# Kernel optimization log

Measured on AMD Instinct MI355X. Metric: run time of the kernel, lower is better.

Reference implementation:

```python
import jax, jax.numpy as jnp
import numpy as np
from jax import lax

B, T_ENC, T_DEC = 512, 64, 64
A = 64            # num_activities (pad token id = A)
ATTR_V = 10       # categorical attr vocab
ATTR_E, ACT_E, CF, ZD = 16, 64, 512, 128
TOT_ATTR = ATTR_E + 1           # 17
TDIM = TOT_ATTR // 2 + CF       # 8 + 512 = 520


def _lin(x, W, b):
    # torch nn.Linear: W is [out, in]
    return x @ W.T + b


def _cell(x, h, c, Wih, Whh, b):
    # torch LSTM cell, gate order i,f,g,o
    g = x @ Wih.T + h @ Whh.T + b
    i, f, gg, o = jnp.split(g, 4, axis=-1)
    c = jax.nn.sigmoid(f) * c + jax.nn.sigmoid(i) * jnp.tanh(gg)
    h = jax.nn.sigmoid(o) * jnp.tanh(c)
    return h, c


def setup_inputs() -> dict:
    key = jax.random.key(0)
    ks = iter(jax.random.split(key, 64))
    def n(shape, s=0.05):
        return jax.random.normal(next(ks), shape, jnp.float32) * s
    rng = np.random.default_rng(0)
    lens = rng.integers(2, T_ENC, size=B)
    acts_np = rng.integers(0, A - 1, size=(B, T_ENC))
    acts_np[np.arange(T_ENC)[None, :] >= lens[:, None]] = A  # pad token (max value -> argmax = len)
    return dict(
        attr_cat=jnp.asarray(rng.integers(0, ATTR_V, size=B), jnp.int32),
        attr_num=jax.random.uniform(next(ks), (B,), jnp.float32),
        acts=jnp.asarray(acts_np, jnp.int32),
        ts=jax.random.uniform(next(ks), (B, T_ENC), jnp.float32),
        epsilon=n((B, ZD), 1.0),
        attr_emb=n((ATTR_V, ATTR_E)),
        a2a_W=n((TOT_ATTR // 2, TOT_ATTR)), a2a_b=n((TOT_ATTR // 2,)),
        act_emb=n((A + 1, ACT_E)).at[A].set(0.0),  # padding_idx row zeroed
        eWih=n((4 * CF, ACT_E + 1)), eWhh=n((4 * CF, CF)), ebih=n((4 * CF,)), ebhh=n((4 * CF,)),
        mean_W=n((ZD, TDIM)), mean_b=n((ZD,)),
        var_W=n((ZD, TDIM)), var_b=n((ZD,)),
        z2t_W=n((TDIM, ZD)), z2t_b=n((TDIM,)),
        tc1_W=n((TDIM // 2, TDIM)), tc1_b=n((TDIM // 2,)),
        tc2_W=n((ATTR_V, TDIM // 2)), tc2_b=n((ATTR_V,)),
        tn1_W=n((TDIM // 2, TDIM)), tn1_b=n((TDIM // 2,)),
        tn2_W=n((1, TDIM // 2)), tn2_b=n((1,)),
        aWih=n((4 * CF, TDIM + ACT_E)), aWhh=n((4 * CF, CF)), abih=n((4 * CF,)), abhh=n((4 * CF,)),
        tWih=n((4 * CF, TDIM + ACT_E + 1)), tWhh=n((4 * CF, CF)), tbih=n((4 * CF,)), tbhh=n((4 * CF,)),
        e2act_W=n((A, CF)), e2act_b=n((A,)),
        ts1_W=n((CF // 2, CF)), ts1_b=n((CF // 2,)),
        ts2_W=n((1, CF // 2)), ts2_b=n((1,)),
    )


def reference(attr_cat, attr_num, acts, ts, epsilon,
              attr_emb, a2a_W, a2a_b, act_emb,
              eWih, eWhh, ebih, ebhh,
              mean_W, mean_b, var_W, var_b,
              z2t_W, z2t_b,
              tc1_W, tc1_b, tc2_W, tc2_b,
              tn1_W, tn1_b, tn2_W, tn2_b,
              aWih, aWhh, abih, abhh,
              tWih, tWhh, tbih, tbhh,
              e2act_W, e2act_b,
              ts1_W, ts1_b, ts2_W, ts2_b):
    # ---------- Encoder ----------
    e_attrs = jnp.concatenate([attr_emb[attr_cat], attr_num[:, None]], axis=1)   # [B,17]
    e_attrs = jax.nn.relu(_lin(e_attrs, a2a_W, a2a_b))                            # [B,8]
    x = jnp.concatenate([act_emb[acts], ts[:, :, None]], axis=2)                  # [B,T,ACT_E+1]
    eb = ebih + ebhh
    def enc_step(carry, xt):
        h, c = carry
        h, c = _cell(xt, h, c, eWih, eWhh, eb)
        return (h, c), h
    h0 = jnp.zeros((x.shape[0], CF), x.dtype)
    _, hs = lax.scan(enc_step, (h0, h0), jnp.swapaxes(x, 0, 1))
    cf_all = jnp.swapaxes(hs, 0, 1)                                               # [B,T,CF]
    # packed-sequence equivalence: LSTM is causal, we only read step lens-1
    lens = jnp.argmax(acts, axis=1)
    cf = cf_all[jnp.arange(cf_all.shape[0]), lens - 1]                            # [B,CF]
    t = jnp.concatenate([e_attrs, cf], axis=1)                                    # [B,TDIM]
    mean = _lin(t, mean_W, mean_b)
    var = _lin(t, var_W, var_b)
    z = mean + var * epsilon                                                      # reparameterization
    # ---------- Decoder ----------
    t_rec = jax.nn.relu(_lin(z, z2t_W, z2t_b))                                    # [B,TDIM]
    attr_cat_rec = jax.nn.softmax(_lin(jax.nn.relu(_lin(t_rec, tc1_W, tc1_b)), tc2_W, tc2_b), axis=1)
    attr_num_rec = jax.nn.sigmoid(_lin(jax.nn.relu(_lin(t_rec, tn1_W, tn1_b)), tn2_W, tn2_b))
    Bsz = t_rec.shape[0]
    ab, tb = abih + abhh, tbih + tbhh
    eot = jnp.broadcast_to(act_emb[A - 1], (Bsz, ACT_E))
    carry0 = (h0, h0, h0, h0, eot, jnp.zeros((Bsz, 1), t_rec.dtype))
    def dec_step(carry, _):
        h_a, c_a, h_t, c_t, ae, tsc = carry
        h_a, c_a = _cell(jnp.concatenate([t_rec, ae], 1), h_a, c_a, aWih, aWhh, ab)
        logits = _lin(h_a, e2act_W, e2act_b)                                      # [B,A]
        ae2 = act_emb[jnp.argmax(logits, axis=1)]                                 # greedy feedback
        h_t, c_t = _cell(jnp.concatenate([t_rec, ae2, tsc], 1), h_t, c_t, tWih, tWhh, tb)
        tsn = _lin(jax.nn.relu(_lin(h_t, ts1_W, ts1_b)), ts2_W, ts2_b)            # [B,1]
        return (h_a, c_a, h_t, c_t, ae2, tsn), (logits, tsn[:, 0])
    _, (logits_all, ts_all) = lax.scan(dec_step, carry0, None, length=T_DEC)
    acts_rec = jax.nn.softmax(jnp.swapaxes(logits_all, 0, 1), axis=2)             # [B,T_DEC,A]
    ts_rec = jnp.swapaxes(ts_all, 0, 1)                                           # [B,T_DEC]
    return (attr_cat_rec, attr_num_rec, acts_rec, ts_rec, mean, var)
```

## Files before the change

### kernel.cpp

```cpp
#include <hip/hip_runtime.h>
#include <math.h>


#define B 512
#define TT 64
#define CF 512
#define G4 2048
#define ZD 128
#define TDIM 520

typedef unsigned short u16;
typedef unsigned int u32;
typedef unsigned long long u64;
typedef short bf16x8 __attribute__((ext_vector_type(8)));
typedef float f32x4 __attribute__((ext_vector_type(4)));

__device__ __forceinline__ float sigm(float x) { return 1.f / (1.f + expf(-x)); }
__device__ __forceinline__ u16 f2bf(float f) {
    unsigned u = __float_as_uint(f);
    u += 0x7fffu + ((u >> 16) & 1u);
    return (u16)(u >> 16);
}
__device__ __forceinline__ float bf2f(u16 s) { return __uint_as_float(((unsigned)s) << 16); }
__device__ __forceinline__ u32 packbf(float v) {
    u16 hh = f2bf(v);
    u16 hl = f2bf(v - bf2f(hh));
    return (u32)hh | ((u32)hl << 16);
}

__device__ __forceinline__ void ast32(u32* p, u32 v) {
    __hip_atomic_store(p, v, __ATOMIC_RELAXED, __HIP_MEMORY_SCOPE_AGENT);
}
__device__ __forceinline__ u64 ald64(const u64* p) {
    return __hip_atomic_load(p, __ATOMIC_RELAXED, __HIP_MEMORY_SCOPE_AGENT);
}
__device__ __forceinline__ void astf(float* p, float v) {
    __hip_atomic_store(p, v, __ATOMIC_RELAXED, __HIP_MEMORY_SCOPE_AGENT);
}
__device__ __forceinline__ float aldf(const float* p) {
    return __hip_atomic_load(p, __ATOMIC_RELAXED, __HIP_MEMORY_SCOPE_AGENT);
}

__device__ __forceinline__ void unpk8(u64 a, u64 b, u64 c, u64 d,
                                      uint4& hi, uint4& lo) {
    u32 a0 = (u32)a, a1 = (u32)(a >> 32);
    u32 b0 = (u32)b, b1 = (u32)(b >> 32);
    u32 c0 = (u32)c, c1 = (u32)(c >> 32);
    u32 d0 = (u32)d, d1 = (u32)(d >> 32);
    hi.x = (a0 & 0xffffu) | (a1 << 16);  lo.x = (a0 >> 16) | (a1 & 0xffff0000u);
    hi.y = (b0 & 0xffffu) | (b1 << 16);  lo.y = (b0 >> 16) | (b1 & 0xffff0000u);
    hi.z = (c0 & 0xffffu) | (c1 << 16);  lo.z = (c0 >> 16) | (c1 & 0xffff0000u);
    hi.w = (d0 & 0xffffu) | (d1 << 16);  lo.w = (d0 >> 16) | (d1 & 0xffff0000u);
}

__device__ __forceinline__ void gsync_fast(int* bar, int target) {
    __syncthreads();
    if (threadIdx.x == 0) {
        __hip_atomic_fetch_add(bar, 1, __ATOMIC_RELEASE, __HIP_MEMORY_SCOPE_AGENT);
        while (__hip_atomic_load(bar, __ATOMIC_RELAXED, __HIP_MEMORY_SCOPE_AGENT) < target)
            __builtin_amdgcn_s_sleep(2);
    }
    __syncthreads();
}

__device__ __forceinline__ void gsync_full(int* bar, int target) {
    __syncthreads();
    if (threadIdx.x == 0) {
        __threadfence();
        __hip_atomic_fetch_add(bar, 1, __ATOMIC_ACQ_REL, __HIP_MEMORY_SCOPE_AGENT);
        while (__hip_atomic_load(bar, __ATOMIC_ACQUIRE, __HIP_MEMORY_SCOPE_AGENT) < target)
            __builtin_amdgcn_s_sleep(2);
        __threadfence();
    }
    __syncthreads();
}

struct __align__(16) GemmShared {
    u16 A[2][2][64][40];
    u16 Bw[2][2][64][40];
};

struct Pref { u64 a0, a1, a2, a3; uint4 bh, bl; };

template<int TERMS>
__device__ __forceinline__ void pf_issue(Pref& p, const u64* xp,
        const u16* wph, const u16* wpl, int it) {
    const int k = it << 5;
    const u64* xq = xp + (k >> 1);
    p.a0 = ald64(xq); p.a1 = ald64(xq + 1);
    p.a2 = ald64(xq + 2); p.a3 = ald64(xq + 3);
    p.bh = *(const uint4*)(wph + k);
    if (TERMS == 3) p.bl = *(const uint4*)(wpl + k);
}

template<int TERMS>
__device__ __forceinline__ void pf_write(GemmShared& sh, const Pref& p,
        int nxt, int srr, int skq) {
    uint4 hi, lo; unpk8(p.a0, p.a1, p.a2, p.a3, hi, lo);
    *(uint4*)&sh.A[nxt][0][srr][skq] = hi;
    *(uint4*)&sh.A[nxt][1][srr][skq] = lo;
    *(uint4*)&sh.Bw[nxt][0][srr][skq] = p.bh;
    if (TERMS == 3) *(uint4*)&sh.Bw[nxt][1][srr][skq] = p.bl;
}

template<int TERMS>
__device__ __forceinline__ void pf_comp(GemmShared& sh, int cur,
        int row, int ko, int fr, f32x4 acc[4]) {
    bf16x8 ah = *(const bf16x8*)&sh.A[cur][0][row][ko];
    bf16x8 al = *(const bf16x8*)&sh.A[cur][1][row][ko];
    #pragma unroll
    for (int nt = 0; nt < 4; ++nt) {
        bf16x8 bh = *(const bf16x8*)&sh.Bw[cur][0][(nt << 4) + fr][ko];
        acc[nt] = __builtin_amdgcn_mfma_f32_16x16x32_bf16(ah, bh, acc[nt], 0, 0, 0);
        if (TERMS == 3) {
            bf16x8 bl = *(const bf16x8*)&sh.Bw[cur][1][(nt << 4) + fr][ko];
            acc[nt] = __builtin_amdgcn_mfma_f32_16x16x32_bf16(ah, bl, acc[nt], 0, 0, 0);
        }
        acc[nt] = __builtin_amdgcn_mfma_f32_16x16x32_bf16(al, bh, acc[nt], 0, 0, 0);
    }
}

template<int TERMS>
__device__ __forceinline__ void gemm64i(
    GemmShared& sh,
    const u32* __restrict__ A32, int lda,
    const u16* __restrict__ Bh, const u16* __restrict__ Bl, int K, int ldb,
    f32x4 acc[4])
{
    const int tid = threadIdx.x;
    const int lane = tid & 63, ws = tid >> 6;
    const int fr = lane & 15, quad = lane >> 4, ko = quad << 3;
    const int srr = tid >> 2, skq = (tid & 3) << 3;
    const int row = (ws << 4) + fr;

    const u64* xp = (const u64*)(A32 + srr * lda + skq);
    const u16* wph = Bh + srr * ldb + skq;
    const u16* wpl = (TERMS == 3) ? (Bl + srr * ldb + skq) : (const u16*)0;

    const int niter = K >> 5;
    {
        u64 d0 = ald64(xp), d1 = ald64(xp + 1), d2 = ald64(xp + 2), d3 = ald64(xp + 3);
        uint4 hi, lo; unpk8(d0, d1, d2, d3, hi, lo);
        *(uint4*)&sh.A[0][0][srr][skq] = hi;
        *(uint4*)&sh.A[0][1][srr][skq] = lo;
        *(uint4*)&sh.Bw[0][0][srr][skq] = *(const uint4*)(wph);
        if (TERMS == 3) *(uint4*)&sh.Bw[0][1][srr][skq] = *(const uint4*)(wpl);
    }
    Pref pA, pB;
    if (niter > 1) pf_issue<TERMS>(pA, xp, wph, wpl, 1);
    if (niter > 2) pf_issue<TERMS>(pB, xp, wph, wpl, 2);
    __syncthreads();

    int i = 0;
    for (;;) {
        pf_comp<TERMS>(sh, 0, row, ko, fr, acc);
        if (i + 1 < niter) {
            pf_write<TERMS>(sh, pA, 1, srr, skq);
            if (i + 3 < niter) pf_issue<TERMS>(pA, xp, wph, wpl, i + 3);
        }
        __syncthreads();
        if (++i >= niter) break;
        pf_comp<TERMS>(sh, 1, row, ko, fr, acc);
        if (i + 1 < niter) {
            pf_write<TERMS>(sh, pB, 0, srr, skq);
            if (i + 3 < niter) pf_issue<TERMS>(pB, xp, wph, wpl, i + 3);
        }
        __syncthreads();
        if (++i >= niter) break;
    }
}

__device__ __forceinline__ void ts_strip(
    GemmShared& sh, const u32* __restrict__ Xt32r,
    const u16* __restrict__ W1h, const float* __restrict__ b1,
    const float* __restrict__ w2, int ncg, float s[4])
{
    const int lane = threadIdx.x & 63;
    const int fr = lane & 15;
    f32x4 ac[4] = {};
    gemm64i<2>(sh, Xt32r, 512, W1h + (size_t)(ncg << 6) * 512, nullptr, 512, 512, ac);
    s[0] = s[1] = s[2] = s[3] = 0.f;
    #pragma unroll
    for (int nt = 0; nt < 4; ++nt) {
        int j = (ncg << 6) + (nt << 4) + fr;
        float b1v = b1[j], w2v = w2[j];
        s[0] += fmaxf(ac[nt][0] + b1v, 0.f) * w2v;
        s[1] += fmaxf(ac[nt][1] + b1v, 0.f) * w2v;
        s[2] += fmaxf(ac[nt][2] + b1v, 0.f) * w2v;
        s[3] += fmaxf(ac[nt][3] + b1v, 0.f) * w2v;
    }
    #pragma unroll
    for (int off = 1; off < 16; off <<= 1) {
        s[0] += __shfl_xor(s[0], off);
        s[1] += __shfl_xor(s[1], off);
        s[2] += __shfl_xor(s[2], off);
        s[3] += __shfl_xor(s[3], off);
    }
}

__global__ __launch_bounds__(256, 1) void enc_coop(
    u32* __restrict__ Xe32,
    const u16* __restrict__ Weh, const u16* __restrict__ Wel,
    const float* __restrict__ biaspk,
    float* __restrict__ tcat, const int* __restrict__ lens,
    const int* __restrict__ acts, const float* __restrict__ tsv,
    const float* __restrict__ act_emb, int* __restrict__ bars)
{
    __shared__ GemmShared sh;
    const int bx = blockIdx.x, by = blockIdx.y, row0 = by << 6;
    const int tid = threadIdx.x, lane = tid & 63, ws = tid >> 6;
    const int fr = lane & 15, quad = lane >> 4;
    const int cell = (bx << 4) + fr;
    const int rbase = row0 + (ws << 4) + (quad << 2);
    int* bar = bars + by * 32;
    int gen = 0;

    float bb[4], ce[4] = {0.f, 0.f, 0.f, 0.f};
    int lm1[4];
    #pragma unroll
    for (int g = 0; g < 4; ++g) bb[g] = biaspk[(bx << 6) + (g << 4) + fr];
    #pragma unroll
    for (int r = 0; r < 4; ++r) lm1[r] = lens[rbase + r] - 1;

    for (int t = 0; t < TT; ++t) {
        const u32* xc = Xe32 + (size_t)(t & 1) * B * 608;
        u32* xn = Xe32 + (size_t)((t + 1) & 1) * B * 608;

        f32x4 acc[4] = {};
        gemm64i<3>(sh, xc + (size_t)row0 * 608, 608,
                   Weh + (size_t)(bx << 6) * 608, Wel + (size_t)(bx << 6) * 608,
                   608, 608, acc);

        #pragma unroll
        for (int r = 0; r < 4; ++r) {
            int b = rbase + r;
            float gi = acc[0][r] + bb[0], gf = acc[1][r] + bb[1];
            float gg = acc[2][r] + bb[2], go = acc[3][r] + bb[3];
            float cn = sigm(gf) * ce[r] + sigm(gi) * tanhf(gg);
            ce[r] = cn;
            float h = sigm(go) * tanhf(cn);
            ast32(&xn[b * 608 + 65 + cell], packbf(h));
            if (t == lm1[r]) tcat[b * TDIM + 8 + cell] = h;
        }
        if (t < TT - 1) {
            for (int idx = tid; idx < 130; idx += 256) {
                int hi2 = (idx >= 65);
                int r = (bx << 1) + hi2, cc = idx - hi2 * 65;
                int b = row0 + r;
                float v = (cc < 64) ? act_emb[acts[(b << 6) + t + 1] * 64 + cc]
                                    : tsv[(b << 6) + t + 1];
                ast32(&xn[b * 608 + cc], packbf(v));
            }
            gsync_fast(bar, (++gen) * 32);
        }
    }
}

__global__ __launch_bounds__(256, 1) void dec_coop(
    u32* __restrict__ Xa32,
    u16* Wah, u16* Wal,
    const float* __restrict__ aWih, const float* __restrict__ aWhh,
    const float* __restrict__ base_a,
    u32* __restrict__ Xt32,
    const u16* __restrict__ Wth, const u16* __restrict__ Wtl,
    const float* __restrict__ base_t,
    const u16* __restrict__ E2h, const u16* __restrict__ E2l,
    const float* __restrict__ e2b, const float* __restrict__ act_emb,
    float* __restrict__ out_acts, float* __restrict__ out_ts,
    const u16* __restrict__ W1h, const float* __restrict__ b1,
    const float* __restrict__ w2, const float* __restrict__ b2p,
    float* __restrict__ tspart, int* __restrict__ bars)
{
    __shared__ GemmShared sh;
    __shared__ u16 ae2h[64][72];
    __shared__ u16 ae2l[64][72];
    const int bx = blockIdx.x, by = blockIdx.y, row0 = by << 6;
    const int tid = threadIdx.x, lane = tid & 63, ws = tid >> 6;
    const int fr = lane & 15, quad = lane >> 4;
    const int srr = tid >> 2, skq = (tid & 3) << 3;
    const bool bx0 = (bx == 0);
    const int cell = (bx << 4) + fr;
    const int rb0 = (ws << 4) + (quad << 2);
    const int rbase = row0 + rb0;
    const float tsb2 = b2p[0];
    int* barG = bars + 512;
    int* bar  = bars + 256 + by * 32;
    int gen = 0;

    {
        const int gtid = (((by << 5) + bx) << 8) + tid;
        for (int idx = gtid; idx < G4 * 576; idx += 32 * 8 * 256) {
            int np = idx / 576, k = idx - np * 576;
            int g = (np & 63) >> 4;
            int n = (g << 9) + (((np >> 6) << 4) + (np & 15));
            float v = (k < 64) ? aWih[n * 584 + 520 + k] : aWhh[(n << 9) + k - 64];
            u16 h = f2bf(v);
            Wah[idx] = h; Wal[idx] = f2bf(v - bf2f(h));
        }
    }

    float e2bv[4];
    float ca_r[4] = {0.f, 0.f, 0.f, 0.f}, ct_r[4] = {0.f, 0.f, 0.f, 0.f};
    #pragma unroll
    for (int nt = 0; nt < 4; ++nt) e2bv[nt] = e2b[(nt << 4) + fr];

    gsync_full(barG, 256);

    for (int t = 0; t < TT; ++t) {
        u32* xac = Xa32 + (size_t)(t & 1) * B * 576;
        u32* xan = Xa32 + (size_t)((t + 1) & 1) * B * 576;
        const u32* xtc = Xt32 + (size_t)(t & 1) * B * 512;
        u32* xtn = Xt32 + (size_t)((t + 1) & 1) * B * 512;

        {
            f32x4 acc[4] = {};
            gemm64i<3>(sh, xac + (size_t)row0 * 576, 576,
                       Wah + (size_t)(bx << 6) * 576, Wal + (size_t)(bx << 6) * 576,
                       576, 576, acc);
            #pragma unroll
            for (int r = 0; r < 4; ++r) {
                int b = rbase + r;
                const float* bp = base_a + (size_t)b * G4 + (bx << 6) + fr;
                float gi = acc[0][r] + bp[0], gf = acc[1][r] + bp[16];
                float gg = acc[2][r] + bp[32], go = acc[3][r] + bp[48];
                float cn = sigm(gf) * ca_r[r] + sigm(gi) * tanhf(gg);
                ca_r[r] = cn;
                float h = sigm(go) * tanhf(cn);
                ast32(&xan[b * 576 + 64 + cell], packbf(h));
            }
            if (bx < 4 && t > 0) {
                float s[4];
                ts_strip(sh, xtc + (size_t)row0 * 512, W1h, b1, w2, bx, s);
                if (fr == 0) {
                    #pragma unroll
                    for (int r = 0; r < 4; ++r) astf(&tspart[(bx << 9) + rbase + r], s[r]);
                }
            }
        }
        gsync_fast(bar, (++gen) * 32);

        if (t > 0 && bx == 1 && tid < 64) {
            int b = row0 + tid;
            out_ts[(b << 6) + t - 1] =
                aldf(&tspart[b]) + aldf(&tspart[512 + b]) +
                aldf(&tspart[1024 + b]) + aldf(&tspart[1536 + b]) + tsb2;
        }
        float tsq = 0.f;
        if (t > 0) {
            int b = row0 + srr;
            tsq = aldf(&tspart[b]) + aldf(&tspart[512 + b]) +
                  aldf(&tspart[1024 + b]) + aldf(&tspart[1536 + b]) + tsb2;
        }
        {
            f32x4 acc[4] = {};
            gemm64i<3>(sh, xan + (size_t)row0 * 576 + 64, 576, E2h, E2l, 512, 512, acc);
            #pragma unroll
            for (int r = 0; r < 4; ++r) {
                float l0 = acc[0][r] + e2bv[0], l1 = acc[1][r] + e2bv[1];
                float l2 = acc[2][r] + e2bv[2], l3 = acc[3][r] + e2bv[3];
                float m = fmaxf(fmaxf(l0, l1), fmaxf(l2, l3));
                #pragma unroll
                for (int off = 1; off < 16; off <<= 1) m = fmaxf(m, __shfl_xor(m, off));
                float e0 = expf(l0 - m), e1 = expf(l1 - m);
                float e2v = expf(l2 - m), e3 = expf(l3 - m);
                float sm = e0 + e1 + e2v + e3;
                #pragma unroll
                for (int off = 1; off < 16; off <<= 1) sm += __shfl_xor(sm, off);
                float bv = l0; int bc = fr;
                if (l1 > bv) { bv = l1; bc = 16 + fr; }
                if (l2 > bv) { bv = l2; bc = 32 + fr; }
                if (l3 > bv) { bv = l3; bc = 48 + fr; }
                #pragma unroll
                for (int off = 1; off < 16; off <<= 1) {
                    float ov = __shfl_xor(bv, off);
                    int oc = __shfl_xor(bc, off);
                    if (ov > bv || (ov == bv && oc < bc)) { bv = ov; bc = oc; }
                }
                int rl = rb0 + r, b = row0 + rl;
                if (bx0) {
                    float inv = 1.f / sm;
                    float* op = out_acts + (((size_t)(b << 6) + t) << 6);
                    op[fr] = e0 * inv; op[16 + fr] = e1 * inv;
                    op[32 + fr] = e2v * inv; op[48 + fr] = e3 * inv;
                }
                #pragma unroll
                for (int ci = 0; ci < 4; ++ci) {
                    int cc = (fr << 2) + ci;
                    float v = act_emb[(bc << 6) + cc];
                    u16 hh = f2bf(v), hl = f2bf(v - bf2f(hh));
                    ae2h[rl][cc] = hh; ae2l[rl][cc] = hl;
                    if (bx0) ast32(&xan[b * 576 + cc], ((u32)hh) | ((u32)hl << 16));
                }
            }
        }
        __syncthreads();

        f32x4 acc[4] = {};
        gemm64i<3>(sh, xtc + (size_t)row0 * 512, 512,
                   Wth + (size_t)(bx << 6) * 608, Wtl + (size_t)(bx << 6) * 608,
                   512, 608, acc);
        {
            const u16* wph = Wth + (size_t)((bx << 6) + srr) * 608 + skq;
            const u16* wpl = Wtl + (size_t)((bx << 6) + srr) * 608 + skq;
            const int ko = quad << 3;
            for (int i = 16; i < 19; ++i) {
                int k0 = i << 5;
                uint4 vh, vl;
                if (i < 18) {
                    int co = k0 - 512 + skq;
                    vh = *(const uint4*)&ae2h[srr][co];
                    vl = *(const uint4*)&ae2l[srr][co];
                } else {
                    union U { uint4 q; u16 s[8]; } uh, ul;
                    uh.q = make_uint4(0, 0, 0, 0); ul.q = make_uint4(0, 0, 0, 0);
                    if (skq == 0) {
                        u16 hh = f2bf(tsq);
                        uh.s[0] = hh; ul.s[0] = f2bf(tsq - bf2f(hh));
                    }
                    vh = uh.q; vl = ul.q;
                }
                uint4 wh = *(const uint4*)(wph + k0);
                uint4 wl = *(const uint4*)(wpl + k0);
                __syncthreads();
                *(uint4*)&sh.A[0][0][srr][skq] = vh;
                *(uint4*)&sh.A[0][1][srr][skq] = vl;
                *(uint4*)&sh.Bw[0][0][srr][skq] = wh;
                *(uint4*)&sh.Bw[0][1][srr][skq] = wl;
                __syncthreads();
                bf16x8 ah = *(const bf16x8*)&sh.A[0][0][(ws << 4) + fr][ko];
                bf16x8 al = *(const bf16x8*)&sh.A[0][1][(ws << 4) + fr][ko];
                #pragma unroll
                for (int nt = 0; nt < 4; ++nt) {
                    bf16x8 bh = *(const bf16x8*)&sh.Bw[0][0][(nt << 4) + fr][ko];
                    bf16x8 bl = *(const bf16x8*)&sh.Bw[0][1][(nt << 4) + fr][ko];
                    acc[nt] = __builtin_amdgcn_mfma_f32_16x16x32_bf16(ah, bh, acc[nt], 0, 0, 0);
                    acc[nt] = __builtin_amdgcn_mfma_f32_16x16x32_bf16(ah, bl, acc[nt], 0, 0, 0);
                    acc[nt] = __builtin_amdgcn_mfma_f32_16x16x32_bf16(al, bh, acc[nt], 0, 0, 0);
                }
            }
        }
        #pragma unroll
        for (int r = 0; r < 4; ++r) {
            int b = rbase + r;
            const float* bp = base_t + (size_t)b * G4 + (bx << 6) + fr;
            float gi = acc[0][r] + bp[0], gf = acc[1][r] + bp[16];
            float gg = acc[2][r] + bp[32], go = acc[3][r] + bp[48];
            float cn = sigm(gf) * ct_r[r] + sigm(gi) * tanhf(gg);
            ct_r[r] = cn;
            float h = sigm(go) * tanhf(cn);
            ast32(&xtn[(b << 9) + cell], packbf(h));
        }
        gsync_fast(bar, (++gen) * 32);
    }

    if (bx < 4) {
        float s[4];
        ts_strip(sh, Xt32 + (size_t)row0 * 512, W1h, b1, w2, bx, s);
        if (fr == 0) {
            #pragma unroll
            for (int r = 0; r < 4; ++r) astf(&tspart[(bx << 9) + rbase + r], s[r]);
        }
    }
    gsync_fast(bar, (++gen) * 32);
    if (bx == 0 && tid < 64) {
        int b = row0 + tid;
        out_ts[(b << 6) + 63] =
            aldf(&tspart[b]) + aldf(&tspart[512 + b]) +
            aldf(&tspart[1024 + b]) + aldf(&tspart[1536 + b]) + tsb2;
    }
}

__device__ __forceinline__ int perm_src(int np) {
    int g = (np & 63) >> 4;
    int cell = ((np >> 6) << 4) + (np & 15);
    return (g << 9) + cell;
}

__global__ __launch_bounds__(256) void gemm_tn(
    const float* __restrict__ A, const float* __restrict__ Am,
    const float* __restrict__ Av, const float* __restrict__ Ae, int lda,
    const float* __restrict__ W1p, int ldw1,
    const float* __restrict__ W2p, int ldw2,
    int N, int K,
    const float* __restrict__ b1p, const float* __restrict__ b2p,
    float* __restrict__ C1, float* __restrict__ C2, int ldc,
    int relu, int permW)
{
    const float* W = W1p; int ldw = ldw1;
    const float* bias = b1p; float* C = C1;
    if (blockIdx.z == 1) { W = W2p; ldw = ldw2; bias = b2p; C = C2; }

    __shared__ __align__(16) float As[32][68];
    __shared__ __align__(16) float Ws[32][68];
    const int tid = threadIdx.x;
    const int tx = tid & 15, ty = tid >> 4;
    const int row0 = blockIdx.y << 6;
    const int col0 = blockIdx.x << 6;

    float acc[4][4] = {};

    for (int k0 = 0; k0 < K; k0 += 32) {
        #pragma unroll
        for (int s = 0; s < 2; ++s) {
            int f = tid + (s << 8);
            int rr = f >> 3;
            int kq = (f & 7) << 2;
            int k = k0 + kq;
            float4 v = make_float4(0.f, 0.f, 0.f, 0.f);
            size_t ro = (size_t)(row0 + rr) * (size_t)lda;
            if (Am) {
                if (k + 3 < K) {
                    float4 m = *(const float4*)(Am + ro + k);
                    float4 vv = *(const float4*)(Av + ro + k);
                    float4 e = *(const float4*)(Ae + ro + k);
                    v.x = fmaf(vv.x, e.x, m.x); v.y = fmaf(vv.y, e.y, m.y);
                    v.z = fmaf(vv.z, e.z, m.z); v.w = fmaf(vv.w, e.w, m.w);
                } else {
                    if (k + 0 < K) v.x = fmaf(Av[ro + k], Ae[ro + k], Am[ro + k]);
                    if (k + 1 < K) v.y = fmaf(Av[ro + k + 1], Ae[ro + k + 1], Am[ro + k + 1]);
                    if (k + 2 < K) v.z = fmaf(Av[ro + k + 2], Ae[ro + k + 2], Am[ro + k + 2]);
                }
            } else {
                const float* ap = A + ro;
                if (k + 3 < K) v = *(const float4*)(ap + k);
                else {
                    if (k + 0 < K) v.x = ap[k + 0];
                    if (k + 1 < K) v.y = ap[k + 1];
                    if (k + 2 < K) v.z = ap[k + 2];
                }
            }
            As[kq + 0][rr] = v.x; As[kq + 1][rr] = v.y;
            As[kq + 2][rr] = v.z; As[kq + 3][rr] = v.w;
        }
        #pragma unroll
        for (int s = 0; s < 2; ++s) {
            int f = tid + (s << 8);
            int rr = f >> 3;
            int kq = (f & 7) << 2;
            int k = k0 + kq;
            int n = col0 + rr;
            float4 v = make_float4(0.f, 0.f, 0.f, 0.f);
            if (n < N) {
                int nsrc = permW ? perm_src(n) : n;
                const float* wp = W + (size_t)nsrc * (size_t)ldw;
                if (k + 3 < K) v = *(const float4*)(wp + k);
                else {
                    if (k + 0 < K) v.x = wp[k + 0];
                    if (k + 1 < K) v.y = wp[k + 1];
                    if (k + 2 < K) v.z = wp[k + 2];
                }
            }
            Ws[kq + 0][rr] = v.x; Ws[kq + 1][rr] = v.y;
            Ws[kq + 2][rr] = v.z; Ws[kq + 3][rr] = v.w;
        }
        __syncthreads();
        #pragma unroll
        for (int k = 0; k < 32; ++k) {
            float4 av = *(const float4*)&As[k][ty << 2];
            float4 bv = *(const float4*)&Ws[k][tx << 2];
            acc[0][0] = fmaf(av.x, bv.x, acc[0][0]);
            acc[0][1] = fmaf(av.x, bv.y, acc[0][1]);
            acc[0][2] = fmaf(av.x, bv.z, acc[0][2]);
            acc[0][3] = fmaf(av.x, bv.w, acc[0][3]);
            acc[1][0] = fmaf(av.y, bv.x, acc[1][0]);
            acc[1][1] = fmaf(av.y, bv.y, acc[1][1]);
            acc[1][2] = fmaf(av.y, bv.z, acc[1][2]);
            acc[1][3] = fmaf(av.y, bv.w, acc[1][3]);
            acc[2][0] = fmaf(av.z, bv.x, acc[2][0]);
            acc[2][1] = fmaf(av.z, bv.y, acc[2][1]);
            acc[2][2] = fmaf(av.z, bv.z, acc[2][2]);
            acc[2][3] = fmaf(av.z, bv.w, acc[2][3]);
            acc[3][0] = fmaf(av.w, bv.x, acc[3][0]);
            acc[3][1] = fmaf(av.w, bv.y, acc[3][1]);
            acc[3][2] = fmaf(av.w, bv.z, acc[3][2]);
            acc[3][3] = fmaf(av.w, bv.w, acc[3][3]);
        }
        __syncthreads();
    }

    #pragma unroll
    for (int i = 0; i < 4; ++i) {
        int rr = row0 + (ty << 2) + i;
        float* cp = C + (size_t)rr * (size_t)ldc;
        #pragma unroll
        for (int j = 0; j < 4; ++j) {
            int cc = col0 + (tx << 2) + j;
            if (cc < N) {
                float v = acc[i][j];
                if (bias) v += bias[cc];
                if (relu) v = fmaxf(v, 0.f);
                cp[cc] = v;
            }
        }
    }
}

#define N_WE (G4 * 608)
#define N_WT (G4 * 608)
#define N_W1 (256 * 512)
#define N_E2 (64 * 512)
__global__ void pack_all(
    u16* __restrict__ Weh, u16* __restrict__ Wel,
    u16* __restrict__ Wth, u16* __restrict__ Wtl,
    u16* __restrict__ W1h,
    u16* __restrict__ E2h, u16* __restrict__ E2l,
    float* __restrict__ be, float* __restrict__ ba, float* __restrict__ bt,
    const float* __restrict__ eWih, const float* __restrict__ eWhh,
    const float* __restrict__ tWih, const float* __restrict__ tWhh,
    const float* __restrict__ ts1W, const float* __restrict__ e2W,
    const float* __restrict__ ebih, const float* __restrict__ ebhh,
    const float* __restrict__ abih, const float* __restrict__ abhh,
    const float* __restrict__ tbih, const float* __restrict__ tbhh)
{
    int idx = blockIdx.x * 256 + threadIdx.x;
    if (idx < N_WE) {
        int np = idx / 608, k = idx - np * 608;
        int n = perm_src(np);
        float v = 0.f;
        if (k < 65) v = eWih[n * 65 + k];
        else if (k < 577) v = eWhh[(n << 9) + k - 65];
        u16 h = f2bf(v); Weh[idx] = h; Wel[idx] = f2bf(v - bf2f(h));
        return;
    }
    idx -= N_WE;
    if (idx < N_WT) {
        int np = idx / 608, k = idx - np * 608;
        int n = perm_src(np);
        float v = 0.f;
        if (k < 512) v = tWhh[(n << 9) + k];
        else if (k < 576) v = tWih[n * 585 + 520 + (k - 512)];
        else if (k == 576) v = tWih[n * 585 + 584];
        u16 h = f2bf(v); Wth[idx] = h; Wtl[idx] = f2bf(v - bf2f(h));
        return;
    }
    idx -= N_WT;
    if (idx < N_W1) {
        W1h[idx] = f2bf(ts1W[idx]);
        return;
    }
    idx -= N_W1;
    if (idx < N_E2) {
        float v = e2W[idx];
        u16 h = f2bf(v); E2h[idx] = h; E2l[idx] = f2bf(v - bf2f(h));
        return;
    }
    idx -= N_E2;
    if (idx < G4) {
        int n = perm_src(idx);
        be[idx] = ebih[n] + ebhh[n];
        ba[idx] = abih[n] + abhh[n];
        bt[idx] = tbih[n] + tbhh[n];
    }
}

__global__ __launch_bounds__(256) void init_all(
    u32* __restrict__ xe0, u32* __restrict__ xe1,
    int* __restrict__ lens, float* __restrict__ tcat,
    u32* __restrict__ xa0, u32* __restrict__ xt0,
    const int* __restrict__ acts, const float* __restrict__ tsv,
    const float* __restrict__ act_emb,
    const int* __restrict__ attr_cat, const float* __restrict__ attr_num,
    const float* __restrict__ attr_emb,
    const float* __restrict__ a2aW, const float* __restrict__ a2ab,
    int* __restrict__ bars)
{
    int b = blockIdx.x, tid = threadIdx.x;
    if (b == 0) {
        for (int j = tid; j < 1024; j += 256)
            __hip_atomic_store(&bars[j], 0, __ATOMIC_RELAXED, __HIP_MEMORY_SCOPE_AGENT);
    }
    for (int j = tid; j < 608; j += 256) {
        float v = 0.f;
        if (j < 64) v = act_emb[acts[b << 6] * 64 + j];
        else if (j == 64) v = tsv[b << 6];
        xe0[b * 608 + j] = packbf(v);
        if (j >= 577) xe1[b * 608 + j] = 0;
    }
    for (int j = tid; j < CF; j += 256) {
        xt0[(b << 9) + j] = 0;
    }
    for (int j = tid; j < 576; j += 256) {
        float v = (j < 64) ? act_emb[63 * 64 + j] : 0.f;
        xa0[b * 576 + j] = packbf(v);
    }
    if (tid < 64) {
        int v = acts[(b << 6) + tid];
        int m = v;
        #pragma unroll
        for (int off = 32; off; off >>= 1) m = max(m, __shfl_xor(m, off));
        unsigned long long mask = __ballot(v == m);
        if (tid == 0) lens[b] = __ffsll(mask) - 1;
    }
    if (tid < 8) {
        const float* wr = a2aW + tid * 17;
        const float* em = attr_emb + attr_cat[b] * 16;
        float s = a2ab[tid];
        #pragma unroll
        for (int k = 0; k < 16; ++k) s = fmaf(em[k], wr[k], s);
        s = fmaf(attr_num[b], wr[16], s);
        tcat[b * TDIM + tid] = fmaxf(s, 0.f);
    }
}

__global__ __launch_bounds__(64) void attr_heads(
    const float* __restrict__ hid1, const float* __restrict__ hid2,
    const float* __restrict__ tc2W, const float* __restrict__ tc2b,
    const float* __restrict__ tn2W, const float* __restrict__ tn2b,
    float* __restrict__ out_cat, float* __restrict__ out_num) {
    __shared__ __align__(16) float h1[260], h2[260], sl[10];
    int b = blockIdx.x, tid = threadIdx.x;
    for (int k = tid; k < 260; k += 64) {
        h1[k] = hid1[b * 260 + k];
        h2[k] = hid2[b * 260 + k];
    }
    __syncthreads();
    if (tid < 10) {
        float l = tc2b[tid];
        const float* wr = tc2W + tid * 260;
        for (int k = 0; k < 260; ++k) l = fmaf(h1[k], wr[k], l);
        sl[tid] = l;
    }
    __syncthreads();
    if (tid < 10) {
        float m = sl[0];
        for (int i = 1; i < 10; ++i) m = fmaxf(m, sl[i]);
        float ssum = 0.f;
        for (int i = 0; i < 10; ++i) ssum += expf(sl[i] - m);
        out_cat[b * 10 + tid] = expf(sl[tid] - m) / ssum;
    }
    float p = 0.f;
    for (int k = tid; k < 260; k += 64) p = fmaf(h2[k], tn2W[k], p);
    #pragma unroll
    for (int off = 32; off; off >>= 1) p += __shfl_xor(p, off);
    if (tid == 0) out_num[b] = 1.f / (1.f + expf(-(p + tn2b[0])));
}

extern "C" void kernel_launch(void* const* d_in, const int* in_sizes, int n_in,
                              void* d_out, int out_size, void* d_ws, size_t ws_size,
                              hipStream_t stream) {
    const int*   attr_cat = (const int*)  d_in[0];
    const float* attr_num = (const float*)d_in[1];
    const int*   acts     = (const int*)  d_in[2];
    const float* tsv      = (const float*)d_in[3];
    const float* eps      = (const float*)d_in[4];
    const float* attr_emb = (const float*)d_in[5];
    const float* a2a_W    = (const float*)d_in[6];
    const float* a2a_b    = (const float*)d_in[7];
    const float* act_emb  = (const float*)d_in[8];
    const float* eWih     = (const float*)d_in[9];
    const float* eWhh     = (const float*)d_in[10];
    const float* ebih     = (const float*)d_in[11];
    const float* ebhh     = (const float*)d_in[12];
    const float* mean_W   = (const float*)d_in[13];
    const float* mean_b   = (const float*)d_in[14];
    const float* var_W    = (const float*)d_in[15];
    const float* var_b    = (const float*)d_in[16];
    const float* z2t_W    = (const float*)d_in[17];
    const float* z2t_b    = (const float*)d_in[18];
    const float* tc1_W    = (const float*)d_in[19];
    const float* tc1_b    = (const float*)d_in[20];
    const float* tc2_W    = (const float*)d_in[21];
    const float* tc2_b    = (const float*)d_in[22];
    const float* tn1_W    = (const float*)d_in[23];
    const float* tn1_b    = (const float*)d_in[24];
    const float* tn2_W    = (const float*)d_in[25];
    const float* tn2_b    = (const float*)d_in[26];
    const float* aWih     = (const float*)d_in[27];
    const float* aWhh     = (const float*)d_in[28];
    const float* abih     = (const float*)d_in[29];
    const float* abhh     = (const float*)d_in[30];
    const float* tWih     = (const float*)d_in[31];
    const float* tWhh     = (const float*)d_in[32];
    const float* tbih     = (const float*)d_in[33];
    const float* tbhh     = (const float*)d_in[34];
    const float* e2act_W  = (const float*)d_in[35];
    const float* e2act_b  = (const float*)d_in[36];
    const float* ts1_W    = (const float*)d_in[37];
    const float* ts1_b    = (const float*)d_in[38];
    const float* ts2_W    = (const float*)d_in[39];
    const float* ts2_b    = (const float*)d_in[40];

    float* out = (float*)d_out;
    float* out_cat  = out;
    float* out_num  = out + 5120;
    float* out_acts = out + 5632;
    float* out_ts   = out + 2102784;
    float* outm     = out + 2135552;
    float* outv     = out + 2201088;

    char* w = (char*)d_ws;
    auto alloc = [&](size_t bytes) { char* p = w; w += (bytes + 255) & ~(size_t)255; return p; };
    u16*   Wt_hi  = (u16*)alloc((size_t)G4 * 608 * 2);
    u16*   Wt_lo  = (u16*)alloc((size_t)G4 * 608 * 2);
    u16*   W1h    = (u16*)alloc(256 * 512 * 2);
    u16*   E2h    = (u16*)alloc(64 * 512 * 2);
    u16*   E2l    = (u16*)alloc(64 * 512 * 2);
    float* bias_e = (float*)alloc(G4 * 4);
    float* bias_a = (float*)alloc(G4 * 4);
    float* bias_t = (float*)alloc(G4 * 4);
    float* base_a = (float*)alloc((size_t)B * G4 * 4);
    float* base_t = (float*)alloc((size_t)B * G4 * 4);
    u32*   Xa32   = (u32*)alloc((size_t)2 * B * 576 * 4);
    u32*   Xt32   = (u32*)alloc((size_t)2 * B * 512 * 4);
    float* tcat   = (float*)alloc((size_t)B * TDIM * 4);
    float* t_rec  = (float*)alloc((size_t)B * TDIM * 4);
    float* hid1   = (float*)alloc((size_t)B * 260 * 4);
    float* hid2   = (float*)alloc((size_t)B * 260 * 4);
    int*   lens   = (int*)alloc(512 * 4);
    float* partial4 = (float*)alloc(4 * 512 * 4);
    int*   bars   = (int*)alloc(4096);
    char* phase = w;
    u16*   We_hi  = (u16*)(phase);
    u16*   We_lo  = (u16*)(phase + (size_t)G4 * 608 * 2);
    u32*   Xe32   = (u32*)(phase + (size_t)2 * G4 * 608 * 2);
    u16*   Wa_hi  = (u16*)(phase);
    u16*   Wa_lo  = (u16*)(phase + (size_t)G4 * 576 * 2);
    (void)ws_size; (void)in_sizes; (void)n_in; (void)out_size;

    {
        int total = N_WE + N_WT + N_W1 + N_E2 + G4;
        pack_all<<<(total + 255) / 256, 256, 0, stream>>>(
            We_hi, We_lo, Wt_hi, Wt_lo, W1h, E2h, E2l,
            bias_e, bias_a, bias_t,
            eWih, eWhh, tWih, tWhh, ts1_W, e2act_W,
            ebih, ebhh, abih, abhh, tbih, tbhh);
    }
    init_all<<<B, 256, 0, stream>>>(
        Xe32, Xe32 + (size_t)B * 608,
        lens, tcat, Xa32, Xt32,
        acts, tsv, act_emb, attr_cat, attr_num, attr_emb, a2a_W, a2a_b,
        bars);

    enc_coop<<<dim3(32, 8), 256, 0, stream>>>(
        Xe32, We_hi, We_lo, bias_e, tcat, lens, acts, tsv, act_emb,
        bars);

    gemm_tn<<<dim3(2, 8, 2), 256, 0, stream>>>(
        tcat, nullptr, nullptr, nullptr, TDIM, mean_W, TDIM, var_W, TDIM,
        ZD, TDIM, mean_b, var_b, outm, outv, ZD, 0, 0);
    gemm_tn<<<dim3(9, 8, 1), 256, 0, stream>>>(
        nullptr, outm, outv, eps, ZD, z2t_W, ZD, nullptr, 0,
        TDIM, ZD, z2t_b, nullptr, t_rec, nullptr, TDIM, 1, 0);
    gemm_tn<<<dim3(5, 8, 2), 256, 0, stream>>>(
        t_rec, nullptr, nullptr, nullptr, TDIM, tc1_W, TDIM, tn1_W, TDIM,
        260, TDIM, tc1_b, tn1_b, hid1, hid2, 260, 1, 0);
    attr_heads<<<B, 64, 0, stream>>>(hid1, hid2, tc2_W, tc2_b, tn2_W, tn2_b, out_cat, out_num);
    gemm_tn<<<dim3(32, 8, 2), 256, 0, stream>>>(
        t_rec, nullptr, nullptr, nullptr, TDIM, aWih, 584, tWih, 585,
        G4, TDIM, bias_a, bias_t, base_a, base_t, G4, 0, 1);

    dec_coop<<<dim3(32, 8), 256, 0, stream>>>(
        Xa32, Wa_hi, Wa_lo, aWih, aWhh, base_a,
        Xt32, Wt_hi, Wt_lo, base_t,
        E2h, E2l, e2act_b, act_emb, out_acts, out_ts,
        W1h, ts1_b, ts2_W, ts2_b, partial4,
        bars);
}
```

Baseline: 4.904 ms.

## Split coop kernels into producer and consumer warps for GEMM tile loads

Doubles the block size of the encoder and decoder cooperative kernels to 512 threads. The upper 256 threads only load global tiles into shared memory and the lower 256 only run MFMA and the LSTM epilogues, so loading and compute are specialised by warp. The aim is to hide global load latency behind the matrix math in the per-step recurrent GEMMs. It costs extra warps and registers per block, and the double-buffer synchronisation is unchanged, so the overlap gained may be limited.

```diff
diff --git a/kernel.cpp b/kernel.cpp
--- a/kernel.cpp
+++ b/kernel.cpp
@@ -128,9 +128,11 @@
     f32x4 acc[4])
 {
     const int tid = threadIdx.x;
-    const int lane = tid & 63, ws = tid >> 6;
+    const bool cons = tid < 256;
+    const int lane = tid & 63, ws = (tid >> 6) & 3;
     const int fr = lane & 15, quad = lane >> 4, ko = quad << 3;
-    const int srr = tid >> 2, skq = (tid & 3) << 3;
+    const int ptid = tid & 255;
+    const int srr = ptid >> 2, skq = (ptid & 3) << 3;
     const int row = (ws << 4) + fr;
 
     const u64* xp = (const u64*)(A32 + srr * lda + skq);
@@ -138,30 +140,32 @@
     const u16* wpl = (TERMS == 3) ? (Bl + srr * ldb + skq) : (const u16*)0;
 
     const int niter = K >> 5;
-    {
+    Pref pA, pB;
+    if (!cons) {
         u64 d0 = ald64(xp), d1 = ald64(xp + 1), d2 = ald64(xp + 2), d3 = ald64(xp + 3);
         uint4 hi, lo; unpk8(d0, d1, d2, d3, hi, lo);
         *(uint4*)&sh.A[0][0][srr][skq] = hi;
         *(uint4*)&sh.A[0][1][srr][skq] = lo;
         *(uint4*)&sh.Bw[0][0][srr][skq] = *(const uint4*)(wph);
         if (TERMS == 3) *(uint4*)&sh.Bw[0][1][srr][skq] = *(const uint4*)(wpl);
-    }
-    Pref pA, pB;
-    if (niter > 1) pf_issue<TERMS>(pA, xp, wph, wpl, 1);
-    if (niter > 2) pf_issue<TERMS>(pB, xp, wph, wpl, 2);
+        if (niter > 1) pf_issue<TERMS>(pA, xp, wph, wpl, 1);
+        if (niter > 2) pf_issue<TERMS>(pB, xp, wph, wpl, 2);
+    }
     __syncthreads();
 
     int i = 0;
     for (;;) {
-        pf_comp<TERMS>(sh, 0, row, ko, fr, acc);
-        if (i + 1 < niter) {
+        if (cons) {
+            pf_comp<TERMS>(sh, 0, row, ko, fr, acc);
+        } else if (i + 1 < niter) {
             pf_write<TERMS>(sh, pA, 1, srr, skq);
             if (i + 3 < niter) pf_issue<TERMS>(pA, xp, wph, wpl, i + 3);
         }
         __syncthreads();
         if (++i >= niter) break;
-        pf_comp<TERMS>(sh, 1, row, ko, fr, acc);
-        if (i + 1 < niter) {
+        if (cons) {
+            pf_comp<TERMS>(sh, 1, row, ko, fr, acc);
+        } else if (i + 1 < niter) {
             pf_write<TERMS>(sh, pB, 0, srr, skq);
             if (i + 3 < niter) pf_issue<TERMS>(pB, xp, wph, wpl, i + 3);
         }
@@ -180,25 +184,27 @@
     f32x4 ac[4] = {};
     gemm64i<2>(sh, Xt32r, 512, W1h + (size_t)(ncg << 6) * 512, nullptr, 512, 512, ac);
     s[0] = s[1] = s[2] = s[3] = 0.f;
-    #pragma unroll
-    for (int nt = 0; nt < 4; ++nt) {
-        int j = (ncg << 6) + (nt << 4) + fr;
-        float b1v = b1[j], w2v = w2[j];
-        s[0] += fmaxf(ac[nt][0] + b1v, 0.f) * w2v;
-        s[1] += fmaxf(ac[nt][1] + b1v, 0.f) * w2v;
-        s[2] += fmaxf(ac[nt][2] + b1v, 0.f) * w2v;
-        s[3] += fmaxf(ac[nt][3] + b1v, 0.f) * w2v;
-    }
-    #pragma unroll
-    for (int off = 1; off < 16; off <<= 1) {
-        s[0] += __shfl_xor(s[0], off);
-        s[1] += __shfl_xor(s[1], off);
-        s[2] += __shfl_xor(s[2], off);
-        s[3] += __shfl_xor(s[3], off);
-    }
-}
-
-__global__ __launch_bounds__(256, 1) void enc_coop(
+    if (threadIdx.x < 256) {
+        #pragma unroll
+        for (int nt = 0; nt < 4; ++nt) {
+            int j = (ncg << 6) + (nt << 4) + fr;
+            float b1v = b1[j], w2v = w2[j];
+            s[0] += fmaxf(ac[nt][0] + b1v, 0.f) * w2v;
+            s[1] += fmaxf(ac[nt][1] + b1v, 0.f) * w2v;
+            s[2] += fmaxf(ac[nt][2] + b1v, 0.f) * w2v;
+            s[3] += fmaxf(ac[nt][3] + b1v, 0.f) * w2v;
+        }
+        #pragma unroll
+        for (int off = 1; off < 16; off <<= 1) {
+            s[0] += __shfl_xor(s[0], off);
+            s[1] += __shfl_xor(s[1], off);
+            s[2] += __shfl_xor(s[2], off);
+            s[3] += __shfl_xor(s[3], off);
+        }
+    }
+}
+
+__global__ __launch_bounds__(512, 1) void enc_coop(
     u32* __restrict__ Xe32,
     const u16* __restrict__ Weh, const u16* __restrict__ Wel,
     const float* __restrict__ biaspk,
@@ -208,7 +214,9 @@
 {
     __shared__ GemmShared sh;
     const int bx = blockIdx.x, by = blockIdx.y, row0 = by << 6;
-    const int tid = threadIdx.x, lane = tid & 63, ws = tid >> 6;
+    const int tid = threadIdx.x;
+    const bool cons = tid < 256;
+    const int lane = tid & 63, ws = (tid >> 6) & 3;
     const int fr = lane & 15, quad = lane >> 4;
     const int cell = (bx << 4) + fr;
     const int rbase = row0 + (ws << 4) + (quad << 2);
@@ -231,19 +239,21 @@
                    Weh + (size_t)(bx << 6) * 608, Wel + (size_t)(bx << 6) * 608,
                    608, 608, acc);
 
-        #pragma unroll
-        for (int r = 0; r < 4; ++r) {
-            int b = rbase + r;
-            float gi = acc[0][r] + bb[0], gf = acc[1][r] + bb[1];
-            float gg = acc[2][r] + bb[2], go = acc[3][r] + bb[3];
-            float cn = sigm(gf) * ce[r] + sigm(gi) * tanhf(gg);
-            ce[r] = cn;
-            float h = sigm(go) * tanhf(cn);
-            ast32(&xn[b * 608 + 65 + cell], packbf(h));
-            if (t == lm1[r]) tcat[b * TDIM + 8 + cell] = h;
+        if (cons) {
+            #pragma unroll
+            for (int r = 0; r < 4; ++r) {
+                int b = rbase + r;
+                float gi = acc[0][r] + bb[0], gf = acc[1][r] + bb[1];
+                float gg = acc[2][r] + bb[2], go = acc[3][r] + bb[3];
+                float cn = sigm(gf) * ce[r] + sigm(gi) * tanhf(gg);
+                ce[r] = cn;
+                float h = sigm(go) * tanhf(cn);
+                ast32(&xn[b * 608 + 65 + cell], packbf(h));
+                if (t == lm1[r]) tcat[b * TDIM + 8 + cell] = h;
+            }
         }
         if (t < TT - 1) {
-            for (int idx = tid; idx < 130; idx += 256) {
+            for (int idx = tid; idx < 130; idx += 512) {
                 int hi2 = (idx >= 65);
                 int r = (bx << 1) + hi2, cc = idx - hi2 * 65;
                 int b = row0 + r;
@@ -256,7 +266,7 @@
     }
 }
 
-__global__ __launch_bounds__(256, 1) void dec_coop(
+__global__ __launch_bounds__(512, 1) void dec_coop(
     u32* __restrict__ Xa32,
     u16* Wah, u16* Wal,
     const float* __restrict__ aWih, const float* __restrict__ aWhh,
@@ -275,9 +285,12 @@
     __shared__ u16 ae2h[64][72];
     __shared__ u16 ae2l[64][72];
     const int bx = blockIdx.x, by = blockIdx.y, row0 = by << 6;
-    const int tid = threadIdx.x, lane = tid & 63, ws = tid >> 6;
+    const int tid = threadIdx.x;
+    const bool cons = tid < 256;
+    const int lane = tid & 63, ws = (tid >> 6) & 3;
     const int fr = lane & 15, quad = lane >> 4;
-    const int srr = tid >> 2, skq = (tid & 3) << 3;
+    const int ptid = tid & 255;
+    const int srr = ptid >> 2, skq = (ptid & 3) << 3;
     const bool bx0 = (bx == 0);
     const int cell = (bx << 4) + fr;
     const int rb0 = (ws << 4) + (quad << 2);
@@ -288,8 +301,8 @@
     int gen = 0;
 
     {
-        const int gtid = (((by << 5) + bx) << 8) + tid;
-        for (int idx = gtid; idx < G4 * 576; idx += 32 * 8 * 256) {
+        const int gtid = (((by << 5) + bx) << 9) + tid;
+        for (int idx = gtid; idx < G4 * 576; idx += 32 * 8 * 512) {
             int np = idx / 576, k = idx - np * 576;
             int g = (np & 63) >> 4;
             int n = (g << 9) + (((np >> 6) << 4) + (np & 15));
@@ -317,21 +330,23 @@
             gemm64i<3>(sh, xac + (size_t)row0 * 576, 576,
                        Wah + (size_t)(bx << 6) * 576, Wal + (size_t)(bx << 6) * 576,
                        576, 576, acc);
-            #pragma unroll
-            for (int r = 0; r < 4; ++r) {
-                int b = rbase + r;
-                const float* bp = base_a + (size_t)b * G4 + (bx << 6) + fr;
-                float gi = acc[0][r] + bp[0], gf = acc[1][r] + bp[16];
-                float gg = acc[2][r] + bp[32], go = acc[3][r] + bp[48];
-                float cn = sigm(gf) * ca_r[r] + sigm(gi) * tanhf(gg);
-                ca_r[r] = cn;
-                float h = sigm(go) * tanhf(cn);
-                ast32(&xan[b * 576 + 64 + cell], packbf(h));
+            if (cons) {
+                #pragma unroll
+                for (int r = 0; r < 4; ++r) {
+                    int b = rbase + r;
+                    const float* bp = base_a + (size_t)b * G4 + (bx << 6) + fr;
+                    float gi = acc[0][r] + bp[0], gf = acc[1][r] + bp[16];
+                    float gg = acc[2][r] + bp[32], go = acc[3][r] + bp[48];
+                    float cn = sigm(gf) * ca_r[r] + sigm(gi) * tanhf(gg);
+                    ca_r[r] = cn;
+                    float h = sigm(go) * tanhf(cn);
+                    ast32(&xan[b * 576 + 64 + cell], packbf(h));
+                }
             }
             if (bx < 4 && t > 0) {
                 float s[4];
                 ts_strip(sh, xtc + (size_t)row0 * 512, W1h, b1, w2, bx, s);
-                if (fr == 0) {
+                if (cons && fr == 0) {
                     #pragma unroll
                     for (int r = 0; r < 4; ++r) astf(&tspart[(bx << 9) + rbase + r], s[r]);
                 }
@@ -354,42 +369,44 @@
         {
             f32x4 acc[4] = {};
             gemm64i<3>(sh, xan + (size_t)row0 * 576 + 64, 576, E2h, E2l, 512, 512, acc);
-            #pragma unroll
-            for (int r = 0; r < 4; ++r) {
-                float l0 = acc[0][r] + e2bv[0], l1 = acc[1][r] + e2bv[1];
-                float l2 = acc[2][r] + e2bv[2], l3 = acc[3][r] + e2bv[3];
-                float m = fmaxf(fmaxf(l0, l1), fmaxf(l2, l3));
+            if (cons) {
                 #pragma unroll
-                for (int off = 1; off < 16; off <<= 1) m = fmaxf(m, __shfl_xor(m, off));
-                float e0 = expf(l0 - m), e1 = expf(l1 - m);
-                float e2v = expf(l2 - m), e3 = expf(l3 - m);
-                float sm = e0 + e1 + e2v + e3;
-                #pragma unroll
-                for (int off = 1; off < 16; off <<= 1) sm += __shfl_xor(sm, off);
-                float bv = l0; int bc = fr;
-                if (l1 > bv) { bv = l1; bc = 16 + fr; }
-                if (l2 > bv) { bv = l2; bc = 32 + fr; }
-                if (l3 > bv) { bv = l3; bc = 48 + fr; }
-                #pragma unroll
-                for (int off = 1; off < 16; off <<= 1) {
-                    float ov = __shfl_xor(bv, off);
-                    int oc = __shfl_xor(bc, off);
-                    if (ov > bv || (ov == bv && oc < bc)) { bv = ov; bc = oc; }
-                }
-                int rl = rb0 + r, b = row0 + rl;
-                if (bx0) {
-                    float inv = 1.f / sm;
-                    float* op = out_acts + (((size_t)(b << 6) + t) << 6);
-                    op[fr] = e0 * inv; op[16 + fr] = e1 * inv;
-                    op[32 + fr] = e2v * inv; op[48 + fr] = e3 * inv;
-                }
-                #pragma unroll
-                for (int ci = 0; ci < 4; ++ci) {
-                    int cc = (fr << 2) + ci;
-                    float v = act_emb[(bc << 6) + cc];
-                    u16 hh = f2bf(v), hl = f2bf(v - bf2f(hh));
-                    ae2h[rl][cc] = hh; ae2l[rl][cc] = hl;
-                    if (bx0) ast32(&xan[b * 576 + cc], ((u32)hh) | ((u32)hl << 16));
+                for (int r = 0; r < 4; ++r) {
+                    float l0 = acc[0][r] + e2bv[0], l1 = acc[1][r] + e2bv[1];
+                    float l2 = acc[2][r] + e2bv[2], l3 = acc[3][r] + e2bv[3];
+                    float m = fmaxf(fmaxf(l0, l1), fmaxf(l2, l3));
+                    #pragma unroll
+                    for (int off = 1; off < 16; off <<= 1) m = fmaxf(m, __shfl_xor(m, off));
+                    float e0 = expf(l0 - m), e1 = expf(l1 - m);
+                    float e2v = expf(l2 - m), e3 = expf(l3 - m);
+                    float sm = e0 + e1 + e2v + e3;
+                    #pragma unroll
+                    for (int off = 1; off < 16; off <<= 1) sm += __shfl_xor(sm, off);
+                    float bv = l0; int bc = fr;
+                    if (l1 > bv) { bv = l1; bc = 16 + fr; }
+                    if (l2 > bv) { bv = l2; bc = 32 + fr; }
+                    if (l3 > bv) { bv = l3; bc = 48 + fr; }
+                    #pragma unroll
+                    for (int off = 1; off < 16; off <<= 1) {
+                        float ov = __shfl_xor(bv, off);
+                        int oc = __shfl_xor(bc, off);
+                        if (ov > bv || (ov == bv && oc < bc)) { bv = ov; bc = oc; }
+                    }
+                    int rl = rb0 + r, b = row0 + rl;
+                    if (bx0) {
+                        float inv = 1.f / sm;
+                        float* op = out_acts + (((size_t)(b << 6) + t) << 6);
+                        op[fr] = e0 * inv; op[16 + fr] = e1 * inv;
+                        op[32 + fr] = e2v * inv; op[48 + fr] = e3 * inv;
+                    }
+                    #pragma unroll
+                    for (int ci = 0; ci < 4; ++ci) {
+                        int cc = (fr << 2) + ci;
+                        float v = act_emb[(bc << 6) + cc];
+                        u16 hh = f2bf(v), hl = f2bf(v - bf2f(hh));
+                        ae2h[rl][cc] = hh; ae2l[rl][cc] = hl;
+                        if (bx0) ast32(&xan[b * 576 + cc], ((u32)hh) | ((u32)hl << 16));
+                    }
                 }
             }
         }
@@ -403,52 +420,60 @@
             const u16* wph = Wth + (size_t)((bx << 6) + srr) * 608 + skq;
             const u16* wpl = Wtl + (size_t)((bx << 6) + srr) * 608 + skq;
             const int ko = quad << 3;
-            for (int i = 16; i < 19; ++i) {
-                int k0 = i << 5;
-                uint4 vh, vl;
-                if (i < 18) {
-                    int co = k0 - 512 + skq;
-                    vh = *(const uint4*)&ae2h[srr][co];
-                    vl = *(const uint4*)&ae2l[srr][co];
-                } else {
-                    union U { uint4 q; u16 s[8]; } uh, ul;
-                    uh.q = make_uint4(0, 0, 0, 0); ul.q = make_uint4(0, 0, 0, 0);
-                    if (skq == 0) {
-                        u16 hh = f2bf(tsq);
-                        uh.s[0] = hh; ul.s[0] = f2bf(tsq - bf2f(hh));
+            for (int it = 16; it < 19; ++it) {
+                int k0 = it << 5;
+                uint4 vh, vl, wh, wl;
+                if (!cons) {
+                    if (it < 18) {
+                        int co = k0 - 512 + skq;
+                        vh = *(const uint4*)&ae2h[srr][co];
+                        vl = *(const uint4*)&ae2l[srr][co];
+                    } else {
+                        union U { uint4 q; u16 s[8]; } uh, ul;
+                        uh.q = make_uint4(0, 0, 0, 0); ul.q = make_uint4(0, 0, 0, 0);
+                        if (skq == 0) {
+                            u16 hh = f2bf(tsq);
+                            uh.s[0] = hh; ul.s[0] = f2bf(tsq - bf2f(hh));
+                        }
+                        vh = uh.q; vl = ul.q;
                     }
-                    vh = uh.q; vl = ul.q;
+                    wh = *(const uint4*)(wph + k0);
+                    wl = *(const uint4*)(wpl + k0);
                 }
-                uint4 wh = *(const uint4*)(wph + k0);
-                uint4 wl = *(const uint4*)(wpl + k0);
                 __syncthreads();
-                *(uint4*)&sh.A[0][0][srr][skq] = vh;
-                *(uint4*)&sh.A[0][1][srr][skq] = vl;
-                *(uint4*)&sh.Bw[0][0][srr][skq] = wh;
-                *(uint4*)&sh.Bw[0][1][srr][skq] = wl;
+                if (!cons) {
+                    *(uint4*)&sh.A[0][0][srr][skq] = vh;
+                    *(uint4*)&sh.A[0][1][srr][skq] = vl;
+                    *(uint4*)&sh.Bw[0][0][srr][skq] = wh;
+                    *(uint4*)&sh.Bw[0][1][srr][skq] = wl;
+                }
                 __syncthreads();
-                bf16x8 ah = *(const bf16x8*)&sh.A[0][0][(ws << 4) + fr][ko];
-                bf16x8 al = *(const bf16x8*)&sh.A[0][1][(ws << 4) + fr][ko];
-                #pragma unroll
-                for (int nt = 0; nt < 4; ++nt) {
-                    bf16x8 bh = *(const bf16x8*)&sh.Bw[0][0][(nt << 4) + fr][ko];
-                    bf16x8 bl = *(const bf16x8*)&sh.Bw[0][1][(nt << 4) + fr][ko];
-                    acc[nt] = __builtin_amdgcn_mfma_f32_16x16x32_bf16(ah, bh, acc[nt], 0, 0, 0);
-                    acc[nt] = __builtin_amdgcn_mfma_f32_16x16x32_bf16(ah, bl, acc[nt], 0, 0, 0);
-                    acc[nt] = __builtin_amdgcn_mfma_f32_16x16x32_bf16(al, bh, acc[nt], 0, 0, 0);
+                if (cons) {
+                    bf16x8 ah = *(const bf16x8*)&sh.A[0][0][(ws << 4) + fr][ko];
+                    bf16x8 al = *(const bf16x8*)&sh.A[0][1][(ws << 4) + fr][ko];
+                    #pragma unroll
+                    for (int nt = 0; nt < 4; ++nt) {
+                        bf16x8 bh = *(const bf16x8*)&sh.Bw[0][0][(nt << 4) + fr][ko];
+                        bf16x8 bl = *(const bf16x8*)&sh.Bw[0][1][(nt << 4) + fr][ko];
+                        acc[nt] = __builtin_amdgcn_mfma_f32_16x16x32_bf16(ah, bh, acc[nt], 0, 0, 0);
+                        acc[nt] = __builtin_amdgcn_mfma_f32_16x16x32_bf16(ah, bl, acc[nt], 0, 0, 0);
+                        acc[nt] = __builtin_amdgcn_mfma_f32_16x16x32_bf16(al, bh, acc[nt], 0, 0, 0);
+                    }
                 }
             }
         }
-        #pragma unroll
-        for (int r = 0; r < 4; ++r) {
-            int b = rbase + r;
-            const float* bp = base_t + (size_t)b * G4 + (bx << 6) + fr;
-            float gi = acc[0][r] + bp[0], gf = acc[1][r] + bp[16];
-            float gg = acc[2][r] + bp[32], go = acc[3][r] + bp[48];
-            float cn = sigm(gf) * ct_r[r] + sigm(gi) * tanhf(gg);
-            ct_r[r] = cn;
-            float h = sigm(go) * tanhf(cn);
-            ast32(&xtn[(b << 9) + cell], packbf(h));
+        if (cons) {
+            #pragma unroll
+            for (int r = 0; r < 4; ++r) {
+                int b = rbase + r;
+                const float* bp = base_t + (size_t)b * G4 + (bx << 6) + fr;
+                float gi = acc[0][r] + bp[0], gf = acc[1][r] + bp[16];
+                float gg = acc[2][r] + bp[32], go = acc[3][r] + bp[48];
+                float cn = sigm(gf) * ct_r[r] + sigm(gi) * tanhf(gg);
+                ct_r[r] = cn;
+                float h = sigm(go) * tanhf(cn);
+                ast32(&xtn[(b << 9) + cell], packbf(h));
+            }
         }
         gsync_fast(bar, (++gen) * 32);
     }
@@ -456,7 +481,7 @@
     if (bx < 4) {
         float s[4];
         ts_strip(sh, Xt32 + (size_t)row0 * 512, W1h, b1, w2, bx, s);
-        if (fr == 0) {
+        if (cons && fr == 0) {
             #pragma unroll
             for (int r = 0; r < 4; ++r) astf(&tspart[(bx << 9) + rbase + r], s[r]);
         }
@@ -831,7 +856,7 @@
         acts, tsv, act_emb, attr_cat, attr_num, attr_emb, a2a_W, a2a_b,
         bars);
 
-    enc_coop<<<dim3(32, 8), 256, 0, stream>>>(
+    enc_coop<<<dim3(32, 8), 512, 0, stream>>>(
         Xe32, We_hi, We_lo, bias_e, tcat, lens, acts, tsv, act_emb,
         bars);
 
@@ -849,7 +874,7 @@
         t_rec, nullptr, nullptr, nullptr, TDIM, aWih, 584, tWih, 585,
         G4, TDIM, bias_a, bias_t, base_a, base_t, G4, 0, 1);
 
-    dec_coop<<<dim3(32, 8), 256, 0, stream>>>(
+    dec_coop<<<dim3(32, 8), 512, 0, stream>>>(
         Xa32, Wa_hi, Wa_lo, aWih, aWhh, base_a,
         Xt32, Wt_hi, Wt_lo, base_t,
         E2h, E2l, e2act_b, act_emb, out_acts, out_ts,
```

Result: faster. 4.753 ms (-3.1%).
